# Kernel tuning notes

Hardware: AMD Instinct MI355X
Metric: run time of the kernel (lower is better)

The kernel has to match this reference:

```python
import jax, jax.numpy as jnp
import numpy as np

N = 262144       # nodes (4096 graphs * graph_deg 64)
E = 4194304      # edges
D = 64           # node_dim
DEPTH = 3
GRAPH_DEG = 64


def gcn_conv(x, W, b, src, dst, w):
    """PyG GCNConv with self-loops + symmetric norm; masked edges have w=0."""
    h = x @ W                                             # [N, D]
    deg = jax.ops.segment_sum(w, dst, num_segments=N) + 1.0  # +1 self-loop
    dinv = jax.lax.rsqrt(deg)                             # deg >= 1
    norm = dinv[src] * w * dinv[dst]                      # [E]
    agg = jax.ops.segment_sum(h[src] * norm[:, None], dst, num_segments=N)
    agg = agg + h * (dinv * dinv)[:, None]                # self-loop term
    return agg + b


def setup_inputs() -> dict:
    key = jax.random.key(0)
    ks = jax.random.split(key, 24)

    def xavier(k, fan_in, fan_out):
        lim = np.sqrt(6.0 / (fan_in + fan_out))
        return jax.random.uniform(k, (fan_in, fan_out), jnp.float32, -lim, lim)

    inp = {
        "x": jax.random.normal(ks[0], (N, 1), jnp.float32),
        "edge_index": jax.random.randint(ks[1], (2, E), 0, N, jnp.int64),
        "edge_types": jax.random.randint(ks[2], (E,), 0, 5, jnp.int64),
        "node_W": xavier(ks[3], 1, D), "node_b": jnp.zeros((D,), jnp.float32),
        "out1_W": xavier(ks[4], D, D), "out1_b": jnp.zeros((D,), jnp.float32),
        "out2_W": xavier(ks[5], D, 1), "out2_b": jnp.zeros((1,), jnp.float32),
    }
    names = ["W1", "W2", "W3", "W4", "W2b", "W3b", "W4b"]
    for i, n in enumerate(names):
        inp[n] = xavier(ks[6 + i], D, D)
        inp["b" + n[1:]] = jnp.zeros((D,), jnp.float32)
    return inp


def reference(x, edge_index, edge_types,
              node_W, node_b,
              W1, b1, W2, b2, W3, b3, W4, b4,
              W2b, b2b, W3b, b3b, W4b, b4b,
              out1_W, out1_b, out2_W, out2_b):
    src, dst = edge_index[0], edge_index[1]
    w1 = (edge_types == 1).astype(jnp.float32)
    w2 = (edge_types == 2).astype(jnp.float32)
    w3 = (edge_types == 3).astype(jnp.float32)
    w4 = (edge_types == 4).astype(jnp.float32)

    h = x @ node_W + node_b                               # [N, D]
    for _ in range(DEPTH):
        h_new = (gcn_conv(h, W1, b1, src, dst, w1)
                 + gcn_conv(h, W2, b2, src, dst, w2)
                 + gcn_conv(h, W3, b3, src, dst, w3)
                 + gcn_conv(h, W4, b4, src, dst, w4)
                 + gcn_conv(h, W2b, b2b, dst, src, w2)    # reversed edges
                 + gcn_conv(h, W3b, b3b, dst, src, w3)
                 + gcn_conv(h, W4b, b4b, dst, src, w4))
        h = jax.nn.relu(h_new)

    g = h.reshape(-1, GRAPH_DEG, D)                       # [B, deg, D]
    g = jnp.max(g, axis=1)                                # [B, D]
    g = jax.nn.relu(g @ out1_W + out1_b)
    return g @ out2_W + out2_b                            # [B, 1]
```

## Files before the change

kernel.cpp:

```cpp
#include <hip/hip_runtime.h>
#include <stdint.h>

typedef unsigned int u32;
typedef unsigned short u16;
typedef __attribute__((ext_vector_type(8))) short bf16x8;
typedef __attribute__((ext_vector_type(4))) float f32x4;

#define BCAP 16384u

struct Ptr7 { const float* p[7]; };

__device__ __forceinline__ int rfl(int v) { return __builtin_amdgcn_readfirstlane(v); }
__device__ __forceinline__ u16 f2bf(float f) {
    u32 u = __float_as_uint(f);
    u32 r = (u + 0x7FFFu + ((u >> 16) & 1u)) >> 16;
    return (u16)r;
}
__device__ __forceinline__ float bf2f(u16 h) { return __uint_as_float((u32)h << 16); }


__global__ void k_init_cur(u32* __restrict__ g) {
    int i = blockIdx.x * 256 + threadIdx.x;
    if (i < 512) g[i] = (u32)i << 14;
}

__global__ __launch_bounds__(256)
void k_passA(const int* __restrict__ ei, const int* __restrict__ ty, int E,
             u32* __restrict__ gcursor, u32* __restrict__ tmpItems) {
    __shared__ u32 hist[512], gb[512], cur[512];
    int tid = threadIdx.x;
    int e0 = blockIdx.x * 4096;
    hist[tid] = 0; hist[tid + 256] = 0;
    __syncthreads();
#pragma unroll
    for (int i = 0; i < 16; i++) {
        int e = e0 + i * 256 + tid;
        if (e < E) {
            int s = ei[e], d = ei[E + e], t = ty[e];
            if (t >= 1) atomicAdd(&hist[(u32)d >> 9], 1u);
            if (t >= 2) atomicAdd(&hist[(u32)s >> 9], 1u);
        }
    }
    __syncthreads();
    u32 h0 = hist[tid], h1 = hist[tid + 256];
    gb[tid] = h0 ? atomicAdd(&gcursor[tid], h0) : 0u;
    gb[tid + 256] = h1 ? atomicAdd(&gcursor[tid + 256], h1) : 0u;
    cur[tid] = 0; cur[tid + 256] = 0;
    __syncthreads();
#pragma unroll
    for (int i = 0; i < 16; i++) {
        int e = e0 + i * 256 + tid;
        if (e < E) {
            int s = ei[e], d = ei[E + e], t = ty[e];
            if (t >= 1) {
                u32 b = (u32)d >> 9;
                u32 slot = atomicAdd(&cur[b], 1u);
                u32 pos = gb[b] + slot;
                if (pos < ((b + 1u) << 14))
                    tmpItems[pos] = (u32)s | ((u32)(t - 1) << 18) | (((u32)d & 511u) << 21);
            }
            if (t >= 2) {
                u32 b = (u32)s >> 9;
                u32 slot = atomicAdd(&cur[b], 1u);
                u32 pos = gb[b] + slot;
                if (pos < ((b + 1u) << 14))
                    tmpItems[pos] = (u32)d | ((u32)(t + 2) << 18) | (((u32)s & 511u) << 21);
            }
        }
    }
}

__global__ __launch_bounds__(256)
void k_passB(const u32* __restrict__ tmpItems, const u32* __restrict__ bucketEnd,
             float* __restrict__ dinv, u16* __restrict__ dinv16,
             u32* __restrict__ kcnt, int N) {
    __shared__ u32 c[512 * 8];
    int b = blockIdx.x, tid = threadIdx.x;
    for (int i = tid; i < 4096; i += 256) c[i] = 0;
    __syncthreads();
    u32 beg = (u32)b << 14;
    u32 end = bucketEnd[b];
    u32 cap = beg + BCAP;
    if (end > cap) end = cap;
    for (u32 i = beg + tid; i < end; i += 256) {
        u32 it = tmpItems[i];
        atomicAdd(&c[(it >> 21) * 8 + ((it >> 18) & 7)], 1u);
    }
    __syncthreads();
    int nodeBase = b << 9;
    for (int i = tid; i < 4096; i += 256) kcnt[(size_t)b * 4096 + i] = c[i];
    for (int l = tid; l < 512; l += 256) {
        int n = nodeBase + l;
#pragma unroll
        for (int k = 0; k < 7; k++) {
            float v = rsqrtf(1.0f + (float)c[l * 8 + k]);
            dinv[k * N + n] = v;
            dinv16[k * N + n] = f2bf(v);
        }
    }
}

__global__ __launch_bounds__(256)
void k_scan1(const u32* __restrict__ kcnt, u32* __restrict__ kofs, u32* __restrict__ bsums) {
    __shared__ u32 lds[256];
    int t = threadIdx.x;
    size_t base = (size_t)blockIdx.x * 8192 + (size_t)t * 32;
    u32 v[32];
    u32 s = 0;
    const uint4* src = (const uint4*)(kcnt + base);
#pragma unroll
    for (int q = 0; q < 8; q++) {
        uint4 c4 = src[q];
        v[q * 4 + 0] = s; s += c4.x;
        v[q * 4 + 1] = s; s += c4.y;
        v[q * 4 + 2] = s; s += c4.z;
        v[q * 4 + 3] = s; s += c4.w;
    }
    lds[t] = s; __syncthreads();
    for (int off = 1; off < 256; off <<= 1) {
        u32 x2 = (t >= off) ? lds[t - off] : 0u;
        __syncthreads();
        lds[t] += x2;
        __syncthreads();
    }
    u32 texcl = lds[t] - s;
    uint4* dst = (uint4*)(kofs + base);
#pragma unroll
    for (int q = 0; q < 8; q++) {
        uint4 o;
        o.x = v[q * 4 + 0] + texcl; o.y = v[q * 4 + 1] + texcl;
        o.z = v[q * 4 + 2] + texcl; o.w = v[q * 4 + 3] + texcl;
        dst[q] = o;
    }
    if (t == 255) bsums[blockIdx.x] = lds[255];
}

__global__ void k_scan2(const u32* __restrict__ bsums, u32* __restrict__ bexcl, int nb) {
    __shared__ u32 lds[256];
    int t = threadIdx.x;
    u32 v = (t < nb) ? bsums[t] : 0u;
    lds[t] = v; __syncthreads();
    for (int off = 1; off < 256; off <<= 1) {
        u32 x2 = (t >= off) ? lds[t - off] : 0u;
        __syncthreads();
        lds[t] += x2;
        __syncthreads();
    }
    if (t < nb) bexcl[t] = lds[t] - v;
}

__global__ __launch_bounds__(256)
void k_scan3(u32* __restrict__ kofs, const u32* __restrict__ bexcl,
             const u32* __restrict__ bsums, u32 M) {
    int t = threadIdx.x;
    size_t base = (size_t)blockIdx.x * 8192 + (size_t)t * 32;
    u32 add = bexcl[blockIdx.x];
    uint4* p4 = (uint4*)(kofs + base);
#pragma unroll
    for (int q = 0; q < 8; q++) {
        uint4 o = p4[q];
        o.x += add; o.y += add; o.z += add; o.w += add;
        p4[q] = o;
    }
    if (blockIdx.x == 255 && t == 255) kofs[M] = add + bsums[255];
}

__global__ __launch_bounds__(256)
void k_passC(const u32* __restrict__ tmpItems, const u32* __restrict__ bucketEnd,
             const u32* __restrict__ kofs, u32* __restrict__ entries) {
    __shared__ u32 cur[4096];
    int b = blockIdx.x, tid = threadIdx.x;
    for (int i = tid; i < 4096; i += 256) cur[i] = kofs[(size_t)b * 4096 + i];
    __syncthreads();
    u32 beg = (u32)b << 14;
    u32 end = bucketEnd[b];
    u32 cap = beg + BCAP;
    if (end > cap) end = cap;
    for (u32 i = beg + tid; i < end; i += 256) {
        u32 it = tmpItems[i];
        u32 p = atomicAdd(&cur[(it >> 21) * 8 + ((it >> 18) & 7)], 1u);
        entries[p] = it & 0x1FFFFFu;
    }
}

__global__ __launch_bounds__(256)
void k_coef_pq(const u32* __restrict__ entries, const u32* __restrict__ kofs,
               const u16* __restrict__ dinv16, const float* __restrict__ dinv,
               const float* __restrict__ x, u16* __restrict__ coef16,
               float* __restrict__ P, float* __restrict__ Q, int N) {
    int i = blockIdx.x * 256 + threadIdx.x;
    u32 beg = kofs[i], end = kofs[i + 1];
    int k = i & 7, n = i >> 3;
    float sP = 0.f, sQ = 0.f;
    for (u32 p = beg; p < end; ++p) {
        u32 src = entries[p] & 0x3FFFFu;
        u16 cb = dinv16[(size_t)k * N + src];
        coef16[p] = cb;
        float cf = bf2f(cb);
        sP += cf * x[src];
        sQ += cf;
    }
    if (k < 7) {
        float dk = dinv[k * N + n];
        float xn = x[n];
        P[i] = dk * (sP + dk * xn);
        Q[i] = dk * (sQ + dk);
    }
}

__global__ void k_bsum(Ptr7 b, float* __restrict__ bsum) {
    int d = threadIdx.x;
    float s = 0.f;
#pragma unroll
    for (int k = 0; k < 7; k++) s += b.p[k][d];
    bsum[d] = s;
}

__global__ void k_uv(const float* __restrict__ nW, const float* __restrict__ nb,
                     Ptr7 W, float* __restrict__ U, float* __restrict__ V) {
    int k = blockIdx.x, d = threadIdx.x;
    const float* Wk = W.p[k];
    float u = 0.f, v = 0.f;
#pragma unroll 8
    for (int j = 0; j < 64; j++) {
        float w = Wk[j * 64 + d];
        u += nW[j] * w;
        v += nb[j] * w;
    }
    U[k * 64 + d] = u;
    V[k * 64 + d] = v;
}

__global__ void k_packW(Ptr7 W, u16* __restrict__ Wp) {
    int k = blockIdx.x;
    int tid = threadIdx.x;
    int ks = tid >> 8, ct = (tid >> 6) & 3, l = tid & 63;
    const float* Wk = W.p[k];
    u16* dst = Wp + (((size_t)(k * 2 + ks) * 4 + ct) * 512 + l * 8);
    int row0 = ks * 32 + (l >> 4) * 8;
    int col = ct * 16 + (l & 15);
#pragma unroll
    for (int i = 0; i < 8; i++) dst[i] = f2bf(Wk[(row0 + i) * 64 + col]);
}

__global__ __launch_bounds__(256)
void k_h1(const float* __restrict__ P, const float* __restrict__ Q,
          const float* __restrict__ U, const float* __restrict__ V,
          const float* __restrict__ bsum, u16* __restrict__ h1) {
    int i = blockIdx.x * 256 + threadIdx.x;
    int n = rfl(i >> 6);
    int d = i & 63;
    float acc = bsum[d];
#pragma unroll
    for (int k = 0; k < 7; k++)
        acc += P[n * 8 + k] * U[k * 64 + d] + Q[n * 8 + k] * V[k * 64 + d];
    h1[((size_t)n << 6) + d] = f2bf(fmaxf(acc, 0.f));
}

#define GACC(PK, CB, HV)                                             \
    {                                                                \
        float cf_ = __uint_as_float((u32)(CB) << 16);                \
        switch ((PK) >> 18) {                                        \
            case 0: a0 = fmaf(cf_, (HV), a0); break;                 \
            case 1: a1 = fmaf(cf_, (HV), a1); break;                 \
            case 2: a2 = fmaf(cf_, (HV), a2); break;                 \
            case 3: a3 = fmaf(cf_, (HV), a3); break;                 \
            case 4: a4 = fmaf(cf_, (HV), a4); break;                 \
            case 5: a5 = fmaf(cf_, (HV), a5); break;                 \
            default: a6 = fmaf(cf_, (HV), a6); break;                \
        }                                                            \
    }

__global__ __launch_bounds__(256)
void k_gather(const u16* __restrict__ h, const u32* __restrict__ entries,
              const u16* __restrict__ coef16, const u32* __restrict__ kofs,
              const float* __restrict__ dinv, u16* __restrict__ m, int N, int c0) {
    int lane = threadIdx.x & 63;
    int nl = blockIdx.x * 4 + (threadIdx.x >> 6);
    int n = c0 + nl;
    u32 beg = (u32)rfl((int)kofs[(size_t)n << 3]);
    u32 end = (u32)rfl((int)kofs[((size_t)n << 3) + 7]);
    float hv = bf2f(h[((size_t)n << 6) + lane]);
    float d0 = dinv[n],         d1 = dinv[N + n],     d2 = dinv[2 * N + n];
    float d3 = dinv[3 * N + n], d4 = dinv[4 * N + n], d5 = dinv[5 * N + n];
    float d6 = dinv[6 * N + n];
    float a0 = d0 * hv, a1 = d1 * hv, a2 = d2 * hv, a3 = d3 * hv;
    float a4 = d4 * hv, a5 = d5 * hv, a6 = d6 * hv;

    u32 base = beg;
    u32 e = 0, cfw = 0;
    if (base + (u32)lane < end) {
        e = entries[base + lane];
        cfw = (u32)coef16[base + lane];
    }
    while (base < end) {
        u32 rem = end - base;
        int cnt = (rem < 64u) ? (int)rem : 64;
        u32 nb2 = base + 64;
        u32 en = 0, cfn = 0;
        if (nb2 + (u32)lane < end) {
            en = entries[nb2 + lane];
            cfn = (u32)coef16[nb2 + lane];
        }
        int j = 0;
        for (; j + 4 <= cnt; j += 4) {
            u32 pk0 = (u32)__builtin_amdgcn_readlane((int)e, j + 0);
            u32 pk1 = (u32)__builtin_amdgcn_readlane((int)e, j + 1);
            u32 pk2 = (u32)__builtin_amdgcn_readlane((int)e, j + 2);
            u32 pk3 = (u32)__builtin_amdgcn_readlane((int)e, j + 3);
            u32 cb0 = (u32)__builtin_amdgcn_readlane((int)cfw, j + 0);
            u32 cb1 = (u32)__builtin_amdgcn_readlane((int)cfw, j + 1);
            u32 cb2 = (u32)__builtin_amdgcn_readlane((int)cfw, j + 2);
            u32 cb3 = (u32)__builtin_amdgcn_readlane((int)cfw, j + 3);
            float h0 = bf2f(h[((size_t)(pk0 & 0x3FFFFu) << 6) + lane]);
            float h1v = bf2f(h[((size_t)(pk1 & 0x3FFFFu) << 6) + lane]);
            float h2v = bf2f(h[((size_t)(pk2 & 0x3FFFFu) << 6) + lane]);
            float h3v = bf2f(h[((size_t)(pk3 & 0x3FFFFu) << 6) + lane]);
            GACC(pk0, cb0, h0)
            GACC(pk1, cb1, h1v)
            GACC(pk2, cb2, h2v)
            GACC(pk3, cb3, h3v)
        }
        for (; j < cnt; ++j) {
            u32 pk = (u32)__builtin_amdgcn_readlane((int)e, j);
            u32 cb = (u32)__builtin_amdgcn_readlane((int)cfw, j);
            float hval = bf2f(h[((size_t)(pk & 0x3FFFFu) << 6) + lane]);
            GACC(pk, cb, hval)
        }
        e = en; cfw = cfn; base = nb2;
    }

    u16* mp = m + (size_t)nl * 448 + lane;
    mp[0]   = f2bf(d0 * a0); mp[64]  = f2bf(d1 * a1); mp[128] = f2bf(d2 * a2);
    mp[192] = f2bf(d3 * a3); mp[256] = f2bf(d4 * a4); mp[320] = f2bf(d5 * a5);
    mp[384] = f2bf(d6 * a6);
}

__global__ __launch_bounds__(256)
void k_gemm(const u16* __restrict__ m, const u16* __restrict__ Wp,
            const float* __restrict__ bsum, u16* __restrict__ hout, int c0) {
    int tid = threadIdx.x;
    int w = tid >> 6, l = tid & 63;
    int nb = blockIdx.x << 6;
    const u16* arow = m + (size_t)(nb + (w << 4) + (l & 15)) * 448 + ((l >> 4) << 3);
    const u16* bp = Wp + (size_t)l * 8;
    f32x4 acc0 = {0,0,0,0}, acc1 = {0,0,0,0}, acc2 = {0,0,0,0}, acc3 = {0,0,0,0};
#pragma unroll
    for (int kk = 0; kk < 14; kk++) {
        bf16x8 a  = *(const bf16x8*)(arow + kk * 32);
        bf16x8 b0 = *(const bf16x8*)(bp + (size_t)(kk * 4 + 0) * 512);
        bf16x8 b1 = *(const bf16x8*)(bp + (size_t)(kk * 4 + 1) * 512);
        bf16x8 b2 = *(const bf16x8*)(bp + (size_t)(kk * 4 + 2) * 512);
        bf16x8 b3 = *(const bf16x8*)(bp + (size_t)(kk * 4 + 3) * 512);
        acc0 = __builtin_amdgcn_mfma_f32_16x16x32_bf16(a, b0, acc0, 0, 0, 0);
        acc1 = __builtin_amdgcn_mfma_f32_16x16x32_bf16(a, b1, acc1, 0, 0, 0);
        acc2 = __builtin_amdgcn_mfma_f32_16x16x32_bf16(a, b2, acc2, 0, 0, 0);
        acc3 = __builtin_amdgcn_mfma_f32_16x16x32_bf16(a, b3, acc3, 0, 0, 0);
    }
    int rl = (l >> 4) << 2, cl = l & 15;
    int rowg = c0 + nb + (w << 4) + rl;
    f32x4 accs[4] = {acc0, acc1, acc2, acc3};
#pragma unroll
    for (int ct = 0; ct < 4; ct++) {
        int col = ct * 16 + cl;
        float bv = bsum[col];
#pragma unroll
        for (int reg = 0; reg < 4; reg++) {
            float vv = fmaxf(accs[ct][reg] + bv, 0.f);
            hout[(size_t)(rowg + reg) * 64 + col] = f2bf(vv);
        }
    }
}

__global__ __launch_bounds__(256)
void k_head(const u16* __restrict__ h, const float* __restrict__ w1,
            const float* __restrict__ b1, const float* __restrict__ w2,
            const float* __restrict__ b2, float* __restrict__ out) {
    __shared__ float gmax[4][64];
    __shared__ float gl[64];
    __shared__ float t1p[4][64];
    int b = blockIdx.x;
    int tid = threadIdx.x;
    int d = tid & 63, rg = tid >> 6;
    const u16* hb = h + (size_t)b * 64 * 64;
    float pm = -1e30f;
#pragma unroll
    for (int i = 0; i < 16; i++) pm = fmaxf(pm, bf2f(hb[(rg * 16 + i) * 64 + d]));
    gmax[rg][d] = pm; __syncthreads();
    if (rg == 0) gl[d] = fmaxf(fmaxf(gmax[0][d], gmax[1][d]), fmaxf(gmax[2][d], gmax[3][d]));
    __syncthreads();
    float s = 0.f;
#pragma unroll
    for (int i = 0; i < 16; i++) { int dd = rg * 16 + i; s += gl[dd] * w1[dd * 64 + d]; }
    t1p[rg][d] = s; __syncthreads();
    if (rg == 0) {
        float t1 = fmaxf(t1p[0][d] + t1p[1][d] + t1p[2][d] + t1p[3][d] + b1[d], 0.f);
        float v = t1 * w2[d];
        for (int off = 32; off; off >>= 1) v += __shfl_down(v, off, 64);
        if (d == 0) out[b] = v + b2[0];
    }
}

extern "C" void kernel_launch(void* const* d_in, const int* in_sizes, int n_in,
                              void* d_out, int out_size, void* d_ws, size_t ws_size,
                              hipStream_t stream) {
    const float* x     = (const float*)d_in[0];
    const int*   ei    = (const int*)d_in[1];
    const int*   ty    = (const int*)d_in[2];
    const float* nodeW = (const float*)d_in[3];
    const float* nodeb = (const float*)d_in[4];
    const float* out1W = (const float*)d_in[5];
    const float* out1b = (const float*)d_in[6];
    const float* out2W = (const float*)d_in[7];
    const float* out2b = (const float*)d_in[8];

    Ptr7 W, B;
    W.p[0] = (const float*)d_in[9];  B.p[0] = (const float*)d_in[10];
    W.p[1] = (const float*)d_in[11]; B.p[1] = (const float*)d_in[12];
    W.p[2] = (const float*)d_in[13]; B.p[2] = (const float*)d_in[14];
    W.p[3] = (const float*)d_in[15]; B.p[3] = (const float*)d_in[16];
    W.p[4] = (const float*)d_in[17]; B.p[4] = (const float*)d_in[18];
    W.p[5] = (const float*)d_in[19]; B.p[5] = (const float*)d_in[20];
    W.p[6] = (const float*)d_in[21]; B.p[6] = (const float*)d_in[22];

    const int N = in_sizes[0];
    const int E = in_sizes[2];

    char* p = (char*)d_ws;
    auto carve = [&](size_t bytes) { void* r = (void*)p; p += (bytes + 255) & ~(size_t)255; return r; };
    u16*   hA       = (u16*)carve((size_t)N * 64 * 2);
    u16*   hB       = (u16*)carve((size_t)N * 64 * 2);
    u32*   entries  = (u32*)carve((size_t)2 * E * 4);
    u16*   coef16   = (u16*)carve((size_t)2 * E * 2);
    float* dinv     = (float*)carve((size_t)7 * N * 4);
    u16*   dinv16   = (u16*)carve((size_t)7 * N * 2);
    u32*   kcnt     = (u32*)carve((size_t)8 * N * 4);
    u32*   kofs     = (u32*)carve(((size_t)8 * N + 1) * 4);
    float* P        = (float*)carve((size_t)N * 8 * 4);
    float* Q        = (float*)carve((size_t)N * 8 * 4);
    float* U        = (float*)carve(7 * 64 * 4);
    float* V        = (float*)carve(7 * 64 * 4);
    float* bsum     = (float*)carve(256);
    u16*   Wp       = (u16*)carve((size_t)7 * 2 * 4 * 512 * 2);
    u32*   gcursor  = (u32*)carve(512 * 4);
    u32*   bsums    = (u32*)carve(1024);
    u32*   bexcl    = (u32*)carve(1024);
    size_t used = (size_t)(p - (char*)d_ws);
    size_t avail = (ws_size > used) ? (ws_size - used) : 0;
    u32*   tmpItems = (u32*)p;
    u16*   m        = (u16*)p;
    size_t chunkNodes = (avail / (448 * 2)) & ~(size_t)63;
    if (chunkNodes < 64) chunkNodes = 64;
    if (chunkNodes > 65536) chunkNodes = 65536;
    if (chunkNodes > (size_t)N) chunkNodes = (size_t)N;
    (void)n_in; (void)out_size;

    k_init_cur<<<2, 256, 0, stream>>>(gcursor);
    k_passA<<<(E + 4095) / 4096, 256, 0, stream>>>(ei, ty, E, gcursor, tmpItems);
    k_passB<<<512, 256, 0, stream>>>(tmpItems, gcursor, dinv, dinv16, kcnt, N);
    k_scan1<<<256, 256, 0, stream>>>(kcnt, kofs, bsums);
    k_scan2<<<1, 256, 0, stream>>>(bsums, bexcl, 256);
    k_scan3<<<256, 256, 0, stream>>>(kofs, bexcl, bsums, (u32)8 * N);
    k_passC<<<512, 256, 0, stream>>>(tmpItems, gcursor, kofs, entries);
    k_coef_pq<<<(8 * N) / 256, 256, 0, stream>>>(entries, kofs, dinv16, dinv, x,
                                                 coef16, P, Q, N);

    k_bsum<<<1, 64, 0, stream>>>(B, bsum);
    k_uv<<<7, 64, 0, stream>>>(nodeW, nodeb, W, U, V);
    k_packW<<<7, 512, 0, stream>>>(W, Wp);

    k_h1<<<(N * 64) / 256, 256, 0, stream>>>(P, Q, U, V, bsum, hA);

    u16* hcur = hA;
    u16* hnext = hB;
    for (int depth = 0; depth < 2; depth++) {
        for (int c0 = 0; c0 < N; c0 += (int)chunkNodes) {
            int cn = (int)(((size_t)(N - c0) < chunkNodes) ? (size_t)(N - c0) : chunkNodes);
            k_gather<<<cn / 4, 256, 0, stream>>>(hcur, entries, coef16, kofs, dinv, m, N, c0);
            k_gemm<<<cn / 64, 256, 0, stream>>>(m, Wp, bsum, hnext, c0);
        }
        u16* t = hcur; hcur = hnext; hnext = t;
    }

    k_head<<<N / 64, 256, 0, stream>>>(hcur, out1W, out1b, out2W, out2b, (float*)d_out);
}
```

Before: 950.2 us.

## Enlarge passA tiles, unroll gather by 8, use nontemporal m stores/loads

Doubles the edges processed per passA block (8192) so fewer blocks do global cursor atomics. Adds an 8-way unrolled gather loop in the aggregation kernel to put more independent h loads in flight. Marks the intermediate m buffer writes and the GEMM's A-operand reads as nontemporal to reduce cache pollution. The changes are unrelated; fewer passA blocks lowers parallelism, and the wider unroll raises register pressure.

New measurement: 949.5 us. No clear change (-0.1%).

```diff
diff --git a/kernel.cpp b/kernel.cpp
--- a/kernel.cpp
+++ b/kernel.cpp
@@ -29,11 +29,11 @@
              u32* __restrict__ gcursor, u32* __restrict__ tmpItems) {
     __shared__ u32 hist[512], gb[512], cur[512];
     int tid = threadIdx.x;
-    int e0 = blockIdx.x * 4096;
+    int e0 = blockIdx.x * 8192;
     hist[tid] = 0; hist[tid + 256] = 0;
     __syncthreads();
 #pragma unroll
-    for (int i = 0; i < 16; i++) {
+    for (int i = 0; i < 32; i++) {
         int e = e0 + i * 256 + tid;
         if (e < E) {
             int s = ei[e], d = ei[E + e], t = ty[e];
@@ -48,7 +48,7 @@
     cur[tid] = 0; cur[tid + 256] = 0;
     __syncthreads();
 #pragma unroll
-    for (int i = 0; i < 16; i++) {
+    for (int i = 0; i < 32; i++) {
         int e = e0 + i * 256 + tid;
         if (e < E) {
             int s = ei[e], d = ei[E + e], t = ty[e];
@@ -303,6 +303,40 @@
             cfn = (u32)coef16[nb2 + lane];
         }
         int j = 0;
+        for (; j + 8 <= cnt; j += 8) {
+            u32 pk0 = (u32)__builtin_amdgcn_readlane((int)e, j + 0);
+            u32 pk1 = (u32)__builtin_amdgcn_readlane((int)e, j + 1);
+            u32 pk2 = (u32)__builtin_amdgcn_readlane((int)e, j + 2);
+            u32 pk3 = (u32)__builtin_amdgcn_readlane((int)e, j + 3);
+            u32 pk4 = (u32)__builtin_amdgcn_readlane((int)e, j + 4);
+            u32 pk5 = (u32)__builtin_amdgcn_readlane((int)e, j + 5);
+            u32 pk6 = (u32)__builtin_amdgcn_readlane((int)e, j + 6);
+            u32 pk7 = (u32)__builtin_amdgcn_readlane((int)e, j + 7);
+            u32 cb0 = (u32)__builtin_amdgcn_readlane((int)cfw, j + 0);
+            u32 cb1 = (u32)__builtin_amdgcn_readlane((int)cfw, j + 1);
+            u32 cb2 = (u32)__builtin_amdgcn_readlane((int)cfw, j + 2);
+            u32 cb3 = (u32)__builtin_amdgcn_readlane((int)cfw, j + 3);
+            u32 cb4 = (u32)__builtin_amdgcn_readlane((int)cfw, j + 4);
+            u32 cb5 = (u32)__builtin_amdgcn_readlane((int)cfw, j + 5);
+            u32 cb6 = (u32)__builtin_amdgcn_readlane((int)cfw, j + 6);
+            u32 cb7 = (u32)__builtin_amdgcn_readlane((int)cfw, j + 7);
+            float h0 = bf2f(h[((size_t)(pk0 & 0x3FFFFu) << 6) + lane]);
+            float h1v = bf2f(h[((size_t)(pk1 & 0x3FFFFu) << 6) + lane]);
+            float h2v = bf2f(h[((size_t)(pk2 & 0x3FFFFu) << 6) + lane]);
+            float h3v = bf2f(h[((size_t)(pk3 & 0x3FFFFu) << 6) + lane]);
+            float h4v = bf2f(h[((size_t)(pk4 & 0x3FFFFu) << 6) + lane]);
+            float h5v = bf2f(h[((size_t)(pk5 & 0x3FFFFu) << 6) + lane]);
+            float h6v = bf2f(h[((size_t)(pk6 & 0x3FFFFu) << 6) + lane]);
+            float h7v = bf2f(h[((size_t)(pk7 & 0x3FFFFu) << 6) + lane]);
+            GACC(pk0, cb0, h0)
+            GACC(pk1, cb1, h1v)
+            GACC(pk2, cb2, h2v)
+            GACC(pk3, cb3, h3v)
+            GACC(pk4, cb4, h4v)
+            GACC(pk5, cb5, h5v)
+            GACC(pk6, cb6, h6v)
+            GACC(pk7, cb7, h7v)
+        }
         for (; j + 4 <= cnt; j += 4) {
             u32 pk0 = (u32)__builtin_amdgcn_readlane((int)e, j + 0);
             u32 pk1 = (u32)__builtin_amdgcn_readlane((int)e, j + 1);
@@ -331,9 +365,13 @@
     }
 
     u16* mp = m + (size_t)nl * 448 + lane;
-    mp[0]   = f2bf(d0 * a0); mp[64]  = f2bf(d1 * a1); mp[128] = f2bf(d2 * a2);
-    mp[192] = f2bf(d3 * a3); mp[256] = f2bf(d4 * a4); mp[320] = f2bf(d5 * a5);
-    mp[384] = f2bf(d6 * a6);
+    __builtin_nontemporal_store(f2bf(d0 * a0), mp);
+    __builtin_nontemporal_store(f2bf(d1 * a1), mp + 64);
+    __builtin_nontemporal_store(f2bf(d2 * a2), mp + 128);
+    __builtin_nontemporal_store(f2bf(d3 * a3), mp + 192);
+    __builtin_nontemporal_store(f2bf(d4 * a4), mp + 256);
+    __builtin_nontemporal_store(f2bf(d5 * a5), mp + 320);
+    __builtin_nontemporal_store(f2bf(d6 * a6), mp + 384);
 }
 
 __global__ __launch_bounds__(256)
@@ -347,7 +385,7 @@
     f32x4 acc0 = {0,0,0,0}, acc1 = {0,0,0,0}, acc2 = {0,0,0,0}, acc3 = {0,0,0,0};
 #pragma unroll
     for (int kk = 0; kk < 14; kk++) {
-        bf16x8 a  = *(const bf16x8*)(arow + kk * 32);
+        bf16x8 a  = __builtin_nontemporal_load((const bf16x8*)(arow + kk * 32));
         bf16x8 b0 = *(const bf16x8*)(bp + (size_t)(kk * 4 + 0) * 512);
         bf16x8 b1 = *(const bf16x8*)(bp + (size_t)(kk * 4 + 1) * 512);
         bf16x8 b2 = *(const bf16x8*)(bp + (size_t)(kk * 4 + 2) * 512);
@@ -456,7 +494,7 @@
     (void)n_in; (void)out_size;
 
     k_init_cur<<<2, 256, 0, stream>>>(gcursor);
-    k_passA<<<(E + 4095) / 4096, 256, 0, stream>>>(ei, ty, E, gcursor, tmpItems);
+    k_passA<<<(E + 8191) / 8192, 256, 0, stream>>>(ei, ty, E, gcursor, tmpItems);
     k_passB<<<512, 256, 0, stream>>>(tmpItems, gcursor, dinv, dinv16, kcnt, N);
     k_scan1<<<256, 256, 0, stream>>>(kcnt, kofs, bsums);
     k_scan2<<<1, 256, 0, stream>>>(bsums, bexcl, 256);
```
